# Kernel tuning notes

Measured on AMD Instinct MI355X. Metric: run time of the kernel, lower is better.

The kernel has to match this reference:

```python
import jax, jax.numpy as jnp
import numpy as np

B, LQ, LKV = 4, 2048, 2048
E, AUG, H = 2048, 1024, 16
DH = E // H
EPS = 1e-6


def setup_inputs() -> dict:
    key = jax.random.key(0)
    ks = jax.random.split(key, 6)
    s = lambda d: 1.0 / np.sqrt(d)
    return {
        "query": jax.random.normal(ks[0], (B, LQ, E), jnp.float32),
        "aug_hidden_state": jax.random.normal(ks[1], (B, LKV, AUG), jnp.float32),
        "aug_mask": jnp.ones((B, LKV), jnp.float32),
        "proj_w": jax.random.normal(ks[2], (E, AUG), jnp.float32) * s(AUG),
        "proj_b": jnp.zeros((E,), jnp.float32),
        "in_proj_w": jax.random.normal(ks[3], (3 * E, E), jnp.float32) * s(E),
        "in_proj_b": jnp.zeros((3 * E,), jnp.float32),
        "out_proj_w": jax.random.normal(ks[4], (E, E), jnp.float32) * s(E),
        "out_proj_b": jnp.zeros((E,), jnp.float32),
        "rms_w": jnp.zeros((E,), jnp.float32),
    }


def reference(query, aug_hidden_state, aug_mask, proj_w, proj_b,
              in_proj_w, in_proj_b, out_proj_w, out_proj_b, rms_w):
    del aug_mask  # asserted but never used by the original forward
    # key and value: two identical Linear calls in the original -> same tensor
    kv = aug_hidden_state @ proj_w.T + proj_b                      # [B,LKV,E]
    wq, wk, wv = jnp.split(in_proj_w, 3, axis=0)
    bq, bk, bv = jnp.split(in_proj_b, 3, axis=0)
    q = (query @ wq.T + bq).reshape(B, LQ, H, DH)
    k = (kv @ wk.T + bk).reshape(B, LKV, H, DH)
    v = (kv @ wv.T + bv).reshape(B, LKV, H, DH)
    scale = 1.0 / np.sqrt(DH)
    scores = jnp.einsum("bqhd,bkhd->bhqk", q * scale, k)           # [B,H,LQ,LKV]
    attn = jax.nn.softmax(scores, axis=-1)
    ctx = jnp.einsum("bhqk,bkhd->bqhd", attn, v).reshape(B, LQ, E)
    attn_out = ctx @ out_proj_w.T + out_proj_b                      # [B,LQ,E]
    # GemmaRMSNorm: fp32 norm, (1 + weight) gain
    x32 = attn_out.astype(jnp.float32)
    normed = x32 * jax.lax.rsqrt(jnp.mean(x32 * x32, axis=-1, keepdims=True) + EPS)
    attn_out = (normed * (1.0 + rms_w)).astype(attn_out.dtype)
    return attn_out + query
```

## Files before the change

kernel.cpp:

```cpp
#include <hip/hip_runtime.h>
#include <hip/hip_bf16.h>
#include <stdint.h>

#define B_   4
#define LQ_  2048
#define LKV_ 2048
#define E_   2048
#define AUG_ 1024
#define H_   16
#define DH_  128

typedef unsigned short u16;
typedef __bf16 bf16x8 __attribute__((ext_vector_type(8)));
typedef float f32x4 __attribute__((ext_vector_type(4)));
typedef float f32x16 __attribute__((ext_vector_type(16)));
typedef int i32x2 __attribute__((ext_vector_type(2)));

__device__ __forceinline__ u16 f2bf(float f) {
  union { float f; unsigned u; } v; v.f = f;
  unsigned r = v.u + 0x7fffu + ((v.u >> 16) & 1u);
  return (u16)(r >> 16);
}
__device__ __forceinline__ unsigned pk2(float a, float b) {
  return (unsigned)f2bf(a) | ((unsigned)f2bf(b) << 16);
}
__device__ __forceinline__ unsigned cvtpk_bf16(float lo, float hi) {
  unsigned r;
  asm("v_cvt_pk_bf16_f32 %0, %1, %2" : "=v"(r) : "v"(lo), "v"(hi));
  return r;
}

#define GLDS(gsrc, ldst)                                                        \
  __builtin_amdgcn_global_load_lds(                                             \
      (__attribute__((address_space(1))) void*)(uintptr_t)(gsrc),               \
      (__attribute__((address_space(3))) void*)(unsigned)(uintptr_t)(ldst),     \
      16, 0, 0)

#define BARRIER()                                   \
  do {                                              \
    asm volatile("" ::: "memory");                  \
    __builtin_amdgcn_s_barrier();                   \
    asm volatile("" ::: "memory");                  \
  } while (0)

__global__ __launch_bounds__(256) void cast_bf16(const float* __restrict__ in,
                                                 u16* __restrict__ out, int n8) {
  int stride = gridDim.x * blockDim.x;
  for (int i = blockIdx.x * blockDim.x + threadIdx.x; i < n8; i += stride) {
    const float4* p = (const float4*)in + (size_t)i * 2;
    float4 a = p[0], b = p[1];
    uint4 o;
    o.x = pk2(a.x, a.y); o.y = pk2(a.z, a.w);
    o.z = pk2(b.x, b.y); o.w = pk2(b.z, b.w);
    ((uint4*)out)[i] = o;
  }
}

template <int OUTF32>
__global__ __launch_bounds__(512, 2) void gemm_bt2(const u16* __restrict__ A,
                                                   const u16* __restrict__ W,
                                                   const float* __restrict__ bias,
                                                   void* __restrict__ Cp,
                                                   int N, int K) {
  __shared__ __align__(16) u16 As[3][256 * 32];
  __shared__ __align__(16) u16 Bs[3][256 * 32];
  const int tid = threadIdx.x;
  const int wave = tid >> 6, lane = tid & 63;
  const int wr = wave >> 2, wc = wave & 3;
  const int g = lane >> 4, r16 = lane & 15;
  const int m0 = blockIdx.y << 8, n0 = blockIdx.x << 8;

  size_t gA[2], gB[2];
  int ldst[2];
#pragma unroll
  for (int i = 0; i < 2; ++i) {
    int c = tid + i * 512;
    int s = c >> 6, w = c & 63;
    int wp = w ^ (((w >> 5) & 1) << 1);
    int grow = s * 16 + (wp >> 2);
    int gcol = (wp & 3) * 8;
    gA[i] = (size_t)(m0 + grow) * K + gcol;
    gB[i] = (size_t)(n0 + grow) * K + gcol;
    ldst[i] = c * 8;
  }
  const int aoff = r16 * 32 + ((g * 8) ^ ((r16 & 8) ? 16 : 0));

  f32x4 acc[8][4];
#pragma unroll
  for (int m = 0; m < 8; ++m)
#pragma unroll
    for (int n = 0; n < 4; ++n) acc[m][n] = (f32x4){0.f, 0.f, 0.f, 0.f};

  const int NT = K >> 5;
#pragma unroll
  for (int i = 0; i < 2; ++i) GLDS(A + gA[i], &As[0][ldst[i]]);
#pragma unroll
  for (int i = 0; i < 2; ++i) GLDS(W + gB[i], &Bs[0][ldst[i]]);
#pragma unroll
  for (int i = 0; i < 2; ++i) GLDS(A + gA[i] + 32, &As[1][ldst[i]]);
#pragma unroll
  for (int i = 0; i < 2; ++i) GLDS(W + gB[i] + 32, &Bs[1][ldst[i]]);

  int cur = 0;
  for (int t = 0; t < NT; ++t) {
    if (t + 1 < NT)
      asm volatile("s_waitcnt vmcnt(4)" ::: "memory");
    else
      asm volatile("s_waitcnt vmcnt(0)" ::: "memory");
    BARRIER();

    const u16* as = As[cur];
    const u16* bs = Bs[cur];
    int nxt = cur + 2; if (nxt >= 3) nxt -= 3;

    bf16x8 bfr[4], af[4];
#pragma unroll
    for (int n = 0; n < 4; ++n)
      bfr[n] = *(const bf16x8*)&bs[wc * 2048 + n * 512 + aoff];
#pragma unroll
    for (int m = 0; m < 4; ++m)
      af[m] = *(const bf16x8*)&as[wr * 4096 + m * 512 + aoff];
    if (t + 2 < NT) {
      size_t k0 = (size_t)(t + 2) * 32;
#pragma unroll
      for (int i = 0; i < 2; ++i) GLDS(A + gA[i] + k0, &As[nxt][ldst[i]]);
    }
    BARRIER();
    __builtin_amdgcn_s_setprio(1);
#pragma unroll
    for (int m = 0; m < 4; ++m)
#pragma unroll
      for (int n = 0; n < 4; ++n)
        acc[m][n] = __builtin_amdgcn_mfma_f32_16x16x32_bf16(af[m], bfr[n], acc[m][n], 0, 0, 0);
    __builtin_amdgcn_s_setprio(0);

    bf16x8 af2[4];
#pragma unroll
    for (int m = 0; m < 4; ++m)
      af2[m] = *(const bf16x8*)&as[wr * 4096 + (m + 4) * 512 + aoff];
    if (t + 2 < NT) {
      size_t k0 = (size_t)(t + 2) * 32;
#pragma unroll
      for (int i = 0; i < 2; ++i) GLDS(W + gB[i] + k0, &Bs[nxt][ldst[i]]);
    }
    BARRIER();
    __builtin_amdgcn_s_setprio(1);
#pragma unroll
    for (int m = 0; m < 4; ++m)
#pragma unroll
      for (int n = 0; n < 4; ++n)
        acc[m + 4][n] = __builtin_amdgcn_mfma_f32_16x16x32_bf16(af2[m], bfr[n], acc[m + 4][n], 0, 0, 0);
    __builtin_amdgcn_s_setprio(0);

    cur = cur + 1; if (cur >= 3) cur -= 3;
  }

  float bv[4];
#pragma unroll
  for (int n = 0; n < 4; ++n)
    bv[n] = bias ? bias[n0 + wc * 64 + n * 16 + r16] : 0.f;
#pragma unroll
  for (int m = 0; m < 8; ++m) {
    int row = m0 + wr * 128 + m * 16 + g * 4;
#pragma unroll
    for (int n = 0; n < 4; ++n) {
      int col = n0 + wc * 64 + n * 16 + r16;
#pragma unroll
      for (int r = 0; r < 4; ++r) {
        float v = acc[m][n][r] + bv[n];
        if (OUTF32)
          ((float*)Cp)[(size_t)(row + r) * N + col] = v;
        else
          ((u16*)Cp)[(size_t)(row + r) * N + col] = f2bf(v);
      }
    }
  }
}

__global__ __launch_bounds__(256) void transpose_v(const u16* __restrict__ v,
                                                   u16* __restrict__ vt) {
  __shared__ __align__(16) u16 t[64][72];
  int tid = threadIdx.x;
  int bh = blockIdx.z, b = bh >> 4, h = bh & 15;
  int kv0 = blockIdx.x << 6, d0 = blockIdx.y << 6;
  int gr = tid & 7, rw = tid >> 3;
#pragma unroll
  for (int p = 0; p < 2; ++p) {
    int row = rw + p * 32;
    uint4 x = *(const uint4*)&v[((size_t)(b * LKV_) + kv0 + row) * E_ + h * DH_ + d0 + gr * 8];
    *(uint4*)&t[row][gr * 8] = x;
  }
  __syncthreads();
#pragma unroll
  for (int p = 0; p < 2; ++p) {
    int d = rw + p * 32;
    u16 tmp[8];
#pragma unroll
    for (int j = 0; j < 8; ++j) tmp[j] = t[gr * 8 + j][d];
    uint4 o;
    o.x = (unsigned)tmp[0] | ((unsigned)tmp[1] << 16);
    o.y = (unsigned)tmp[2] | ((unsigned)tmp[3] << 16);
    o.z = (unsigned)tmp[4] | ((unsigned)tmp[5] << 16);
    o.w = (unsigned)tmp[6] | ((unsigned)tmp[7] << 16);
    *(uint4*)&vt[(((size_t)(b * H_ + h)) * DH_ + d0 + d) * LKV_ + kv0 + gr * 8] = o;
  }
}

__global__ __launch_bounds__(256) void attn_kernel(const u16* __restrict__ Q,
                                                   const u16* __restrict__ K,
                                                   const u16* __restrict__ Vt,
                                                   u16* __restrict__ Octx) {
  __shared__ __align__(16) u16 Ks[2][64 * 128];
  __shared__ __align__(16) u16 Vs[2][128 * 64];
  const int tid = threadIdx.x, wave = tid >> 6, lane = tid & 63;
  const int bid = blockIdx.x;
  const int qb = bid & 15, bh = bid >> 4, b = bh >> 4, h = bh & 15;
  const int q0 = qb << 7;
  const int l31 = lane & 31, hi = lane >> 5;
  const float Cs = 0.08838834764831845f * 1.4426950408889634f;

  const u16* Qp = Q + ((size_t)(b * LQ_ + q0 + wave * 32 + l31)) * E_ + h * DH_;
  const u16* Kp = K + ((size_t)(b * LKV_)) * E_ + h * DH_;
  const u16* Vp = Vt + (size_t)bh * DH_ * LKV_;

  const int kl_row = lane >> 4, kl_g = lane & 15;
  const int vl_row = lane >> 3, vl_g = lane & 7;

  bf16x8 qf[8];
#pragma unroll
  for (int c = 0; c < 8; ++c) {
    bf16x8 raw = *(const bf16x8*)&Qp[c * 16 + hi * 8];
#pragma unroll
    for (int j = 0; j < 8; ++j) qf[c][j] = (__bf16)((float)raw[j] * Cs);
  }

  bf16x8 VONES;
#pragma unroll
  for (int j = 0; j < 8; ++j) VONES[j] = (__bf16)1.0f;
  f32x16 FZERO = {};

  f32x16 o[4];
#pragma unroll
  for (int d = 0; d < 4; ++d)
#pragma unroll
    for (int r = 0; r < 16; ++r) o[d][r] = 0.f;
  f32x16 ol = {};

  auto STAGE = [&](int kv0, int buf) {
#pragma unroll
    for (int j = 0; j < 4; ++j) {
      int cc = wave * 4 + j;
      int krow = cc * 4 + kl_row;
      GLDS(Kp + (size_t)(kv0 + krow) * E_ + ((kl_g ^ (krow & 15)) << 3), &Ks[buf][cc * 512]);
      int vrow = cc * 8 + vl_row;
      GLDS(Vp + (size_t)vrow * LKV_ + kv0 + ((vl_g ^ (vrow & 7)) << 3), &Vs[buf][cc * 512]);
    }
  };

  const int NT = LKV_ / 64;
  STAGE(0, 0);

  for (int t = 0; t < NT; ++t) {
    const int cur = t & 1;
    if (t + 1 < NT) {
      STAGE((t + 1) * 64, cur ^ 1);
      asm volatile("s_waitcnt vmcnt(8)" ::: "memory");
    } else {
      asm volatile("s_waitcnt vmcnt(0)" ::: "memory");
    }
    BARRIER();

    const u16* ks = Ks[cur];
    const u16* vs = Vs[cur];

    f32x16 st[2];
#pragma unroll
    for (int n = 0; n < 2; ++n) {
      int row = n * 32 + l31;
      bf16x8 kf = *(const bf16x8*)&ks[row * 128 + ((hi ^ (row & 15)) << 3)];
      st[n] = __builtin_amdgcn_mfma_f32_32x32x16_bf16(kf, qf[0], FZERO, 0, 0, 0);
    }
#pragma unroll
    for (int c = 1; c < 8; ++c) {
#pragma unroll
      for (int n = 0; n < 2; ++n) {
        int row = n * 32 + l31;
        bf16x8 kf = *(const bf16x8*)&ks[row * 128 + (((c * 2 + hi) ^ (row & 15)) << 3)];
        st[n] = __builtin_amdgcn_mfma_f32_32x32x16_bf16(kf, qf[c], st[n], 0, 0, 0);
      }
    }

    unsigned AF[4][4];
#pragma unroll
    for (int n = 0; n < 2; ++n) {
      float pv[16];
#pragma unroll
      for (int r = 0; r < 16; ++r) pv[r] = exp2f(st[n][r]);
      unsigned a0 = cvtpk_bf16(pv[0], pv[1]),   a1 = cvtpk_bf16(pv[2], pv[3]);
      unsigned a2 = cvtpk_bf16(pv[4], pv[5]),   a3 = cvtpk_bf16(pv[6], pv[7]);
      unsigned b0 = cvtpk_bf16(pv[8], pv[9]),   b1 = cvtpk_bf16(pv[10], pv[11]);
      unsigned b2 = cvtpk_bf16(pv[12], pv[13]), b3 = cvtpk_bf16(pv[14], pv[15]);
      i32x2 r02 = __builtin_amdgcn_permlane32_swap((int)a0, (int)a2, false, false);
      i32x2 r13 = __builtin_amdgcn_permlane32_swap((int)a1, (int)a3, false, false);
      AF[n * 2][0] = (unsigned)r02[0]; AF[n * 2][1] = (unsigned)r13[0];
      AF[n * 2][2] = (unsigned)r02[1]; AF[n * 2][3] = (unsigned)r13[1];
      i32x2 s02 = __builtin_amdgcn_permlane32_swap((int)b0, (int)b2, false, false);
      i32x2 s13 = __builtin_amdgcn_permlane32_swap((int)b1, (int)b3, false, false);
      AF[n * 2 + 1][0] = (unsigned)s02[0]; AF[n * 2 + 1][1] = (unsigned)s13[0];
      AF[n * 2 + 1][2] = (unsigned)s02[1]; AF[n * 2 + 1][3] = (unsigned)s13[1];
    }

#pragma unroll
    for (int s = 0; s < 4; ++s) {
      union { unsigned u[4]; bf16x8 v; } pk;
      pk.u[0] = AF[s][0]; pk.u[1] = AF[s][1]; pk.u[2] = AF[s][2]; pk.u[3] = AF[s][3];
      bf16x8 pa = pk.v;
#pragma unroll
      for (int db = 0; db < 4; ++db) {
        int d = db * 32 + l31;
        bf16x8 vf = *(const bf16x8*)&vs[d * 64 + (((s * 2 + hi) ^ (d & 7)) << 3)];
        o[db] = __builtin_amdgcn_mfma_f32_32x32x16_bf16(pa, vf, o[db], 0, 0, 0);
      }
      ol = __builtin_amdgcn_mfma_f32_32x32x16_bf16(pa, VONES, ol, 0, 0, 0);
    }
    BARRIER();
  }

#pragma unroll
  for (int r = 0; r < 16; ++r) {
    int crow = (r & 3) + 8 * (r >> 2) + 4 * hi;
    float li = 1.0f / ol[r];
    size_t rb = ((size_t)(b * LQ_ + q0 + wave * 32 + crow)) * E_ + h * DH_ + l31;
#pragma unroll
    for (int db = 0; db < 4; ++db)
      Octx[rb + db * 32] = f2bf(o[db][r] * li);
  }
}

__global__ __launch_bounds__(256) void rms_res(const float* __restrict__ x,
                                               const float* __restrict__ w,
                                               const float* __restrict__ qres,
                                               float* __restrict__ out) {
  int row = blockIdx.x, tid = threadIdx.x;
  const float4* xr = (const float4*)(x + (size_t)row * E_);
  const float4* qr = (const float4*)(qres + (size_t)row * E_);
  const float4* wr4 = (const float4*)w;
  float4 v0 = xr[tid * 2], v1 = xr[tid * 2 + 1];
  float ss = v0.x * v0.x + v0.y * v0.y + v0.z * v0.z + v0.w * v0.w +
             v1.x * v1.x + v1.y * v1.y + v1.z * v1.z + v1.w * v1.w;
  ss += __shfl_xor(ss, 1);  ss += __shfl_xor(ss, 2);
  ss += __shfl_xor(ss, 4);  ss += __shfl_xor(ss, 8);
  ss += __shfl_xor(ss, 16); ss += __shfl_xor(ss, 32);
  __shared__ float ls[4];
  if ((tid & 63) == 0) ls[tid >> 6] = ss;
  __syncthreads();
  float total = ls[0] + ls[1] + ls[2] + ls[3];
  float rs = rsqrtf(total * (1.0f / (float)E_) + 1e-6f);
  float4 q0 = qr[tid * 2], q1 = qr[tid * 2 + 1];
  float4 w0 = wr4[tid * 2], w1 = wr4[tid * 2 + 1];
  float4 o0, o1;
  o0.x = v0.x * rs * (1.f + w0.x) + q0.x;
  o0.y = v0.y * rs * (1.f + w0.y) + q0.y;
  o0.z = v0.z * rs * (1.f + w0.z) + q0.z;
  o0.w = v0.w * rs * (1.f + w0.w) + q0.w;
  o1.x = v1.x * rs * (1.f + w1.x) + q1.x;
  o1.y = v1.y * rs * (1.f + w1.y) + q1.y;
  o1.z = v1.z * rs * (1.f + w1.z) + q1.z;
  o1.w = v1.w * rs * (1.f + w1.w) + q1.w;
  float4* op = (float4*)(out + (size_t)row * E_);
  op[tid * 2] = o0;
  op[tid * 2 + 1] = o1;
}

extern "C" void kernel_launch(void* const* d_in, const int* in_sizes, int n_in,
                              void* d_out, int out_size, void* d_ws, size_t ws_size,
                              hipStream_t stream) {
  const float* query = (const float*)d_in[0];
  const float* aug   = (const float*)d_in[1];
  const float* projw = (const float*)d_in[3];
  const float* projb = (const float*)d_in[4];
  const float* ipw   = (const float*)d_in[5];
  const float* ipb   = (const float*)d_in[6];
  const float* opw   = (const float*)d_in[7];
  const float* opb   = (const float*)d_in[8];
  const float* rmsw  = (const float*)d_in[9];

  char* ws = (char*)d_ws;
  size_t off = 0;
  auto alloc = [&](size_t bytes) {
    void* p = ws + off;
    off += (bytes + 1023) & ~(size_t)1023;
    return p;
  };
  u16* query_bf = (u16*)alloc((size_t)B_ * LQ_ * E_ * 2);
  u16* aug_bf   = (u16*)alloc((size_t)B_ * LKV_ * AUG_ * 2);
  u16* projw_bf = (u16*)alloc((size_t)E_ * AUG_ * 2);
  u16* w_bf     = (u16*)alloc((size_t)3 * E_ * E_ * 2);
  u16* outw_bf  = (u16*)alloc((size_t)E_ * E_ * 2);
  u16* kv_bf    = (u16*)alloc((size_t)B_ * LKV_ * E_ * 2);
  u16* q_bf     = (u16*)alloc((size_t)B_ * LQ_ * E_ * 2);
  u16* k_bf     = (u16*)alloc((size_t)B_ * LKV_ * E_ * 2);
  u16* v_bf     = (u16*)alloc((size_t)B_ * LKV_ * E_ * 2);
  u16* ctx_bf   = (u16*)alloc((size_t)B_ * LQ_ * E_ * 2);
  float* attn_out = (float*)query_bf;
  u16* vt_bf = kv_bf;
  (void)in_sizes; (void)n_in; (void)ws_size;

  const int M = B_ * LQ_;

  cast_bf16<<<1024, 256, 0, stream>>>(query, query_bf, (int)((size_t)M * E_ / 8));
  cast_bf16<<<1024, 256, 0, stream>>>(aug, aug_bf, (int)((size_t)M * AUG_ / 8));
  cast_bf16<<<512, 256, 0, stream>>>(projw, projw_bf, (int)((size_t)E_ * AUG_ / 8));
  cast_bf16<<<1024, 256, 0, stream>>>(ipw, w_bf, (int)((size_t)3 * E_ * E_ / 8));
  cast_bf16<<<512, 256, 0, stream>>>(opw, outw_bf, (int)((size_t)E_ * E_ / 8));

  gemm_bt2<0><<<dim3(E_ / 256, M / 256), 512, 0, stream>>>(aug_bf, projw_bf, projb, kv_bf, E_, AUG_);
  gemm_bt2<0><<<dim3(E_ / 256, M / 256), 512, 0, stream>>>(query_bf, w_bf, ipb, q_bf, E_, E_);
  gemm_bt2<0><<<dim3(E_ / 256, M / 256), 512, 0, stream>>>(kv_bf, w_bf + (size_t)E_ * E_, ipb + E_, k_bf, E_, E_);
  gemm_bt2<0><<<dim3(E_ / 256, M / 256), 512, 0, stream>>>(kv_bf, w_bf + (size_t)2 * E_ * E_, ipb + 2 * E_, v_bf, E_, E_);
  transpose_v<<<dim3(LKV_ / 64, DH_ / 64, B_ * H_), 256, 0, stream>>>(v_bf, vt_bf);
  attn_kernel<<<B_ * H_ * (LQ_ / 128), 256, 0, stream>>>(q_bf, k_bf, vt_bf, ctx_bf);
  gemm_bt2<1><<<dim3(E_ / 256, M / 256), 512, 0, stream>>>(ctx_bf, outw_bf, opb, attn_out, E_, E_);
  rms_res<<<M, 256, 0, stream>>>(attn_out, rmsw, query, (float*)d_out);
}
```

Baseline: 560.3 us.

## Shrink attention KV tile for higher occupancy and emit bf16 out-proj output

The attention kernel now stages 32 KV rows per iteration instead of 64, which halves LDS use and the score registers, and it asks for 4 blocks per CU through launch bounds. Separately, the output projection GEMM writes bf16 instead of fp32, and the RMSNorm/residual kernel reads bf16, which halves that intermediate traffic. The cost is twice as many loop iterations and barriers in attention, and extra rounding of the pre-norm activations to bf16.

```diff
diff --git a/kernel.cpp b/kernel.cpp
--- a/kernel.cpp
+++ b/kernel.cpp
@@ -23,6 +23,9 @@
 }
 __device__ __forceinline__ unsigned pk2(float a, float b) {
   return (unsigned)f2bf(a) | ((unsigned)f2bf(b) << 16);
+}
+__device__ __forceinline__ float bf2f(u16 u) {
+  union { unsigned u; float f; } v; v.u = (unsigned)u << 16; return v.f;
 }
 __device__ __forceinline__ unsigned cvtpk_bf16(float lo, float hi) {
   unsigned r;
@@ -206,12 +209,12 @@
   }
 }
 
-__global__ __launch_bounds__(256) void attn_kernel(const u16* __restrict__ Q,
-                                                   const u16* __restrict__ K,
-                                                   const u16* __restrict__ Vt,
-                                                   u16* __restrict__ Octx) {
-  __shared__ __align__(16) u16 Ks[2][64 * 128];
-  __shared__ __align__(16) u16 Vs[2][128 * 64];
+__global__ __launch_bounds__(256, 4) void attn_kernel(const u16* __restrict__ Q,
+                                                      const u16* __restrict__ K,
+                                                      const u16* __restrict__ Vt,
+                                                      u16* __restrict__ Octx) {
+  __shared__ __align__(16) u16 Ks[2][32 * 128];
+  __shared__ __align__(16) u16 Vs[2][128 * 32];
   const int tid = threadIdx.x, wave = tid >> 6, lane = tid & 63;
   const int bid = blockIdx.x;
   const int qb = bid & 15, bh = bid >> 4, b = bh >> 4, h = bh & 15;
@@ -224,7 +227,7 @@
   const u16* Vp = Vt + (size_t)bh * DH_ * LKV_;
 
   const int kl_row = lane >> 4, kl_g = lane & 15;
-  const int vl_row = lane >> 3, vl_g = lane & 7;
+  const int vl_row = lane >> 2, vl_g = lane & 3;
 
   bf16x8 qf[8];
 #pragma unroll
@@ -248,23 +251,23 @@
 
   auto STAGE = [&](int kv0, int buf) {
 #pragma unroll
-    for (int j = 0; j < 4; ++j) {
-      int cc = wave * 4 + j;
+    for (int j = 0; j < 2; ++j) {
+      int cc = wave * 2 + j;
       int krow = cc * 4 + kl_row;
       GLDS(Kp + (size_t)(kv0 + krow) * E_ + ((kl_g ^ (krow & 15)) << 3), &Ks[buf][cc * 512]);
-      int vrow = cc * 8 + vl_row;
-      GLDS(Vp + (size_t)vrow * LKV_ + kv0 + ((vl_g ^ (vrow & 7)) << 3), &Vs[buf][cc * 512]);
+      int vrow = cc * 16 + vl_row;
+      GLDS(Vp + (size_t)vrow * LKV_ + kv0 + ((vl_g ^ (vrow & 3)) << 3), &Vs[buf][cc * 512]);
     }
   };
 
-  const int NT = LKV_ / 64;
+  const int NT = LKV_ / 32;
   STAGE(0, 0);
 
   for (int t = 0; t < NT; ++t) {
     const int cur = t & 1;
     if (t + 1 < NT) {
-      STAGE((t + 1) * 64, cur ^ 1);
-      asm volatile("s_waitcnt vmcnt(8)" ::: "memory");
+      STAGE((t + 1) * 32, cur ^ 1);
+      asm volatile("s_waitcnt vmcnt(4)" ::: "memory");
     } else {
       asm volatile("s_waitcnt vmcnt(0)" ::: "memory");
     }
@@ -273,52 +276,40 @@
     const u16* ks = Ks[cur];
     const u16* vs = Vs[cur];
 
-    f32x16 st[2];
-#pragma unroll
-    for (int n = 0; n < 2; ++n) {
-      int row = n * 32 + l31;
-      bf16x8 kf = *(const bf16x8*)&ks[row * 128 + ((hi ^ (row & 15)) << 3)];
-      st[n] = __builtin_amdgcn_mfma_f32_32x32x16_bf16(kf, qf[0], FZERO, 0, 0, 0);
-    }
+    bf16x8 kf0 = *(const bf16x8*)&ks[l31 * 128 + ((hi ^ (l31 & 15)) << 3)];
+    f32x16 st = __builtin_amdgcn_mfma_f32_32x32x16_bf16(kf0, qf[0], FZERO, 0, 0, 0);
 #pragma unroll
     for (int c = 1; c < 8; ++c) {
-#pragma unroll
-      for (int n = 0; n < 2; ++n) {
-        int row = n * 32 + l31;
-        bf16x8 kf = *(const bf16x8*)&ks[row * 128 + (((c * 2 + hi) ^ (row & 15)) << 3)];
-        st[n] = __builtin_amdgcn_mfma_f32_32x32x16_bf16(kf, qf[c], st[n], 0, 0, 0);
-      }
-    }
-
-    unsigned AF[4][4];
-#pragma unroll
-    for (int n = 0; n < 2; ++n) {
-      float pv[16];
-#pragma unroll
-      for (int r = 0; r < 16; ++r) pv[r] = exp2f(st[n][r]);
-      unsigned a0 = cvtpk_bf16(pv[0], pv[1]),   a1 = cvtpk_bf16(pv[2], pv[3]);
-      unsigned a2 = cvtpk_bf16(pv[4], pv[5]),   a3 = cvtpk_bf16(pv[6], pv[7]);
-      unsigned b0 = cvtpk_bf16(pv[8], pv[9]),   b1 = cvtpk_bf16(pv[10], pv[11]);
-      unsigned b2 = cvtpk_bf16(pv[12], pv[13]), b3 = cvtpk_bf16(pv[14], pv[15]);
-      i32x2 r02 = __builtin_amdgcn_permlane32_swap((int)a0, (int)a2, false, false);
-      i32x2 r13 = __builtin_amdgcn_permlane32_swap((int)a1, (int)a3, false, false);
-      AF[n * 2][0] = (unsigned)r02[0]; AF[n * 2][1] = (unsigned)r13[0];
-      AF[n * 2][2] = (unsigned)r02[1]; AF[n * 2][3] = (unsigned)r13[1];
-      i32x2 s02 = __builtin_amdgcn_permlane32_swap((int)b0, (int)b2, false, false);
-      i32x2 s13 = __builtin_amdgcn_permlane32_swap((int)b1, (int)b3, false, false);
-      AF[n * 2 + 1][0] = (unsigned)s02[0]; AF[n * 2 + 1][1] = (unsigned)s13[0];
-      AF[n * 2 + 1][2] = (unsigned)s02[1]; AF[n * 2 + 1][3] = (unsigned)s13[1];
-    }
-
-#pragma unroll
-    for (int s = 0; s < 4; ++s) {
+      bf16x8 kf = *(const bf16x8*)&ks[l31 * 128 + (((c * 2 + hi) ^ (l31 & 15)) << 3)];
+      st = __builtin_amdgcn_mfma_f32_32x32x16_bf16(kf, qf[c], st, 0, 0, 0);
+    }
+
+    float pv[16];
+#pragma unroll
+    for (int r = 0; r < 16; ++r) pv[r] = exp2f(st[r]);
+    unsigned a0 = cvtpk_bf16(pv[0], pv[1]),   a1 = cvtpk_bf16(pv[2], pv[3]);
+    unsigned a2 = cvtpk_bf16(pv[4], pv[5]),   a3 = cvtpk_bf16(pv[6], pv[7]);
+    unsigned b0 = cvtpk_bf16(pv[8], pv[9]),   b1 = cvtpk_bf16(pv[10], pv[11]);
+    unsigned b2 = cvtpk_bf16(pv[12], pv[13]), b3 = cvtpk_bf16(pv[14], pv[15]);
+    i32x2 r02 = __builtin_amdgcn_permlane32_swap((int)a0, (int)a2, false, false);
+    i32x2 r13 = __builtin_amdgcn_permlane32_swap((int)a1, (int)a3, false, false);
+    i32x2 s02 = __builtin_amdgcn_permlane32_swap((int)b0, (int)b2, false, false);
+    i32x2 s13 = __builtin_amdgcn_permlane32_swap((int)b1, (int)b3, false, false);
+    unsigned AF[2][4];
+    AF[0][0] = (unsigned)r02[0]; AF[0][1] = (unsigned)r13[0];
+    AF[0][2] = (unsigned)r02[1]; AF[0][3] = (unsigned)r13[1];
+    AF[1][0] = (unsigned)s02[0]; AF[1][1] = (unsigned)s13[0];
+    AF[1][2] = (unsigned)s02[1]; AF[1][3] = (unsigned)s13[1];
+
+#pragma unroll
+    for (int s = 0; s < 2; ++s) {
       union { unsigned u[4]; bf16x8 v; } pk;
       pk.u[0] = AF[s][0]; pk.u[1] = AF[s][1]; pk.u[2] = AF[s][2]; pk.u[3] = AF[s][3];
       bf16x8 pa = pk.v;
 #pragma unroll
       for (int db = 0; db < 4; ++db) {
         int d = db * 32 + l31;
-        bf16x8 vf = *(const bf16x8*)&vs[d * 64 + (((s * 2 + hi) ^ (d & 7)) << 3)];
+        bf16x8 vf = *(const bf16x8*)&vs[d * 32 + (((s * 2 + hi) ^ (d & 3)) << 3)];
         o[db] = __builtin_amdgcn_mfma_f32_32x32x16_bf16(pa, vf, o[db], 0, 0, 0);
       }
       ol = __builtin_amdgcn_mfma_f32_32x32x16_bf16(pa, VONES, ol, 0, 0, 0);
@@ -337,17 +328,20 @@
   }
 }
 
-__global__ __launch_bounds__(256) void rms_res(const float* __restrict__ x,
-                                               const float* __restrict__ w,
-                                               const float* __restrict__ qres,
-                                               float* __restrict__ out) {
+__global__ __launch_bounds__(256) void rms_res_bf(const u16* __restrict__ x,
+                                                  const float* __restrict__ w,
+                                                  const float* __restrict__ qres,
+                                                  float* __restrict__ out) {
   int row = blockIdx.x, tid = threadIdx.x;
-  const float4* xr = (const float4*)(x + (size_t)row * E_);
-  const float4* qr = (const float4*)(qres + (size_t)row * E_);
-  const float4* wr4 = (const float4*)w;
-  float4 v0 = xr[tid * 2], v1 = xr[tid * 2 + 1];
-  float ss = v0.x * v0.x + v0.y * v0.y + v0.z * v0.z + v0.w * v0.w +
-             v1.x * v1.x + v1.y * v1.y + v1.z * v1.z + v1.w * v1.w;
+  uint4 xv = ((const uint4*)(x + (size_t)row * E_))[tid];
+  float xf[8];
+  xf[0] = bf2f((u16)(xv.x & 0xffff)); xf[1] = bf2f((u16)(xv.x >> 16));
+  xf[2] = bf2f((u16)(xv.y & 0xffff)); xf[3] = bf2f((u16)(xv.y >> 16));
+  xf[4] = bf2f((u16)(xv.z & 0xffff)); xf[5] = bf2f((u16)(xv.z >> 16));
+  xf[6] = bf2f((u16)(xv.w & 0xffff)); xf[7] = bf2f((u16)(xv.w >> 16));
+  float ss = 0.f;
+#pragma unroll
+  for (int j = 0; j < 8; ++j) ss += xf[j] * xf[j];
   ss += __shfl_xor(ss, 1);  ss += __shfl_xor(ss, 2);
   ss += __shfl_xor(ss, 4);  ss += __shfl_xor(ss, 8);
   ss += __shfl_xor(ss, 16); ss += __shfl_xor(ss, 32);
@@ -356,17 +350,19 @@
   __syncthreads();
   float total = ls[0] + ls[1] + ls[2] + ls[3];
   float rs = rsqrtf(total * (1.0f / (float)E_) + 1e-6f);
+  const float4* qr = (const float4*)(qres + (size_t)row * E_);
+  const float4* wr4 = (const float4*)w;
   float4 q0 = qr[tid * 2], q1 = qr[tid * 2 + 1];
   float4 w0 = wr4[tid * 2], w1 = wr4[tid * 2 + 1];
   float4 o0, o1;
-  o0.x = v0.x * rs * (1.f + w0.x) + q0.x;
-  o0.y = v0.y * rs * (1.f + w0.y) + q0.y;
-  o0.z = v0.z * rs * (1.f + w0.z) + q0.z;
-  o0.w = v0.w * rs * (1.f + w0.w) + q0.w;
-  o1.x = v1.x * rs * (1.f + w1.x) + q1.x;
-  o1.y = v1.y * rs * (1.f + w1.y) + q1.y;
-  o1.z = v1.z * rs * (1.f + w1.z) + q1.z;
-  o1.w = v1.w * rs * (1.f + w1.w) + q1.w;
+  o0.x = xf[0] * rs * (1.f + w0.x) + q0.x;
+  o0.y = xf[1] * rs * (1.f + w0.y) + q0.y;
+  o0.z = xf[2] * rs * (1.f + w0.z) + q0.z;
+  o0.w = xf[3] * rs * (1.f + w0.w) + q0.w;
+  o1.x = xf[4] * rs * (1.f + w1.x) + q1.x;
+  o1.y = xf[5] * rs * (1.f + w1.y) + q1.y;
+  o1.z = xf[6] * rs * (1.f + w1.z) + q1.z;
+  o1.w = xf[7] * rs * (1.f + w1.w) + q1.w;
   float4* op = (float4*)(out + (size_t)row * E_);
   op[tid * 2] = o0;
   op[tid * 2 + 1] = o1;
@@ -402,7 +398,7 @@
   u16* k_bf     = (u16*)alloc((size_t)B_ * LKV_ * E_ * 2);
   u16* v_bf     = (u16*)alloc((size_t)B_ * LKV_ * E_ * 2);
   u16* ctx_bf   = (u16*)alloc((size_t)B_ * LQ_ * E_ * 2);
-  float* attn_out = (float*)query_bf;
+  u16* attn_out = query_bf;
   u16* vt_bf = kv_bf;
   (void)in_sizes; (void)n_in; (void)ws_size;
 
@@ -420,6 +416,6 @@
   gemm_bt2<0><<<dim3(E_ / 256, M / 256), 512, 0, stream>>>(kv_bf, w_bf + (size_t)2 * E_ * E_, ipb + 2 * E_, v_bf, E_, E_);
   transpose_v<<<dim3(LKV_ / 64, DH_ / 64, B_ * H_), 256, 0, stream>>>(v_bf, vt_bf);
   attn_kernel<<<B_ * H_ * (LQ_ / 128), 256, 0, stream>>>(q_bf, k_bf, vt_bf, ctx_bf);
-  gemm_bt2<1><<<dim3(E_ / 256, M / 256), 512, 0, stream>>>(ctx_bf, outw_bf, opb, attn_out, E_, E_);
-  rms_res<<<M, 256, 0, stream>>>(attn_out, rmsw, query, (float*)d_out);
-}
+  gemm_bt2<0><<<dim3(E_ / 256, M / 256), 512, 0, stream>>>(ctx_bf, outw_bf, opb, attn_out, E_, E_);
+  rms_res_bf<<<M, 256, 0, stream>>>(attn_out, rmsw, query, (float*)d_out);
+}
```

Measured after the change: 811.5 us. 44.8% more time.
